# Optimization experiments

Hardware: AMD Instinct MI355X
Metric: run time of the kernel (lower is better)

Reference implementation:

```python
import jax, jax.numpy as jnp
import numpy as np

ALPHA = 0.2  # LeakyReLU negative slope
OUT_FEATURES = 128


def setup_inputs() -> dict:
    key = jax.random.key(0)
    k1, k2, k3 = jax.random.split(key, 3)
    B, N, F_in, F_out = 4, 4096, 128, OUT_FEATURES
    h = jax.random.normal(k1, (B, N, F_in), dtype=jnp.float32)
    # xavier_uniform with gain 1.414: bound = gain * sqrt(6/(fan_in+fan_out))
    bw = 1.414 * np.sqrt(6.0 / (F_in + F_out))
    W = jax.random.uniform(k2, (F_in, F_out), minval=-bw, maxval=bw, dtype=jnp.float32)
    ba = 1.414 * np.sqrt(6.0 / (2 * F_out + 1))
    a = jax.random.uniform(k3, (2 * F_out, 1), minval=-ba, maxval=ba, dtype=jnp.float32)
    return {"h": h, "W": W, "a": a}


def reference(h, W, a):
    # Wh: [B, N, F_out]
    Wh = jnp.einsum("bni,ij->bnj", h, W)
    a1 = a[:OUT_FEATURES, :]   # [F_out, 1]
    a2 = a[OUT_FEATURES:, :]   # [F_out, 1]
    Wh1 = jnp.einsum("bni,ij->bnj", Wh, a1)  # [B, N, 1]
    Wh2 = jnp.einsum("bni,ij->bnj", Wh, a2)  # [B, N, 1]
    # e: [B, N, N] via broadcast add of column + row vectors
    e = Wh1 + jnp.swapaxes(Wh2, 1, 2)
    e = jax.nn.leaky_relu(e, negative_slope=ALPHA)
    attention = jax.nn.softmax(e, axis=2)
    # dropout is identity in eval mode (p=0.0 / training=False)
    h_prime = jnp.einsum("bij,bjn->bin", attention, Wh)
    return jax.nn.elu(h_prime)
```

## Files before the change

### kernel.cpp

```cpp
#include <hip/hip_runtime.h>
#include <hip/hip_bf16.h>


#define ALPHA 0.2f
#define NN 4096
#define FD 128

typedef __attribute__((ext_vector_type(8))) short s8v;
typedef __attribute__((ext_vector_type(4))) float f4v;
typedef __attribute__((ext_vector_type(2))) unsigned int u2v;
typedef __attribute__((ext_vector_type(4))) unsigned int u4v;

__device__ __forceinline__ unsigned short f2bf(float x) {
  return (unsigned short)((__float_as_uint(x) + 0x8000u) >> 16);
}

__global__ __launch_bounds__(256, 4) void k1_gemm(
    const float* __restrict__ h, const float* __restrict__ W,
    const float* __restrict__ a,
    unsigned short* __restrict__ WhTt,
    float* __restrict__ s1g, float* __restrict__ Eg, float* __restrict__ Fg)
{
  __shared__ __align__(16) unsigned char wls[32768];
  const int tid = threadIdx.x;
  const int b = blockIdx.x >> 6;
  const int j0 = (blockIdx.x & 63) << 6;

#pragma unroll
  for (int it = 0; it < 16; ++it) {
    int cidx = it * 256 + tid;
    int i = cidx >> 5;
    int f0 = (cidx & 31) << 2;
    f4v v = *(const f4v*)(W + (size_t)cidx * 4);
#pragma unroll
    for (int e = 0; e < 4; ++e) {
      int f = f0 + e;
      int byte = f * 256 + (((i >> 3) ^ (f & 15)) << 4) + ((i & 7) << 1);
      *(unsigned short*)(wls + byte) = f2bf(v[e]);
    }
  }
  __syncthreads();

  const int w = tid >> 6, lane = tid & 63;
  const int quad = lane >> 4, lcol = lane & 15;
  const int jrow = j0 + 16 * w + lcol;

  f4v acc[8];
#pragma unroll
  for (int nt = 0; nt < 8; ++nt) acc[nt] = (f4v){0.f, 0.f, 0.f, 0.f};

#pragma unroll
  for (int kk = 0; kk < 4; ++kk) {
    const float* hp = h + (((size_t)(b * NN + jrow)) << 7) + (kk << 5) + (quad << 3);
    f4v v0 = *(const f4v*)hp;
    f4v v1 = *(const f4v*)(hp + 4);
    s8v af;
#pragma unroll
    for (int e = 0; e < 4; ++e) { af[e] = (short)f2bf(v0[e]); af[4+e] = (short)f2bf(v1[e]); }
#pragma unroll
    for (int nt = 0; nt < 8; ++nt) {
      int f = 16 * nt + lcol;
      int slot = ((kk << 2) + quad) ^ (f & 15);
      s8v bfr = *(const s8v*)(wls + (f << 8) + (slot << 4));
      acc[nt] = __builtin_amdgcn_mfma_f32_16x16x32_bf16(af, bfr, acc[nt], 0, 0, 0);
    }
  }

  float s1v[4] = {0,0,0,0}, s2v[4] = {0,0,0,0};
#pragma unroll
  for (int nt = 0; nt < 8; ++nt) {
    float a1 = a[16 * nt + lcol];
    float a2 = a[128 + 16 * nt + lcol];
#pragma unroll
    for (int r = 0; r < 4; ++r) { s1v[r] += acc[nt][r] * a1; s2v[r] += acc[nt][r] * a2; }
  }
#pragma unroll
  for (int r = 0; r < 4; ++r)
#pragma unroll
    for (int d = 1; d < 16; d <<= 1) {
      s1v[r] += __shfl_xor(s1v[r], d, 64);
      s2v[r] += __shfl_xor(s2v[r], d, 64);
    }
  if (lcol == 0) {
    int jb = b * NN + j0 + 16 * w + (quad << 2);
    *(f4v*)(s1g + jb) = (f4v){s1v[0], s1v[1], s1v[2], s1v[3]};
    f4v Ee, Ff;
#pragma unroll
    for (int r = 0; r < 4; ++r) {
      float d = s2v[r] - 8.0f;
      Ee[r] = __expf(d);
      Ff[r] = __expf(ALPHA * d);
    }
    *(f4v*)(Eg + jb) = Ee;
    *(f4v*)(Fg + jb) = Ff;
  }

  {
    const int c = j0 >> 8;
    const int octb = ((j0 & 255) >> 3) + 2 * w + (quad >> 1);
    const int eoff = (quad & 1) << 2;
#pragma unroll
    for (int nt = 0; nt < 8; ++nt) {
      int f = 16 * nt + lcol;
      unsigned u0 = __float_as_uint(acc[nt][0]) + 0x8000u;
      unsigned u1 = __float_as_uint(acc[nt][1]) + 0x8000u;
      unsigned u2 = __float_as_uint(acc[nt][2]) + 0x8000u;
      unsigned u3 = __float_as_uint(acc[nt][3]) + 0x8000u;
      u2v pk;
      pk[0] = (u0 >> 16) | (u1 & 0xFFFF0000u);
      pk[1] = (u2 >> 16) | (u3 & 0xFFFF0000u);
      size_t off = ((((size_t)(b * 16 + c) * 32 + octb) * 128 + f) << 3) + eoff;
      *(u2v*)(WhTt + off) = pk;
    }
  }
}

__global__ __launch_bounds__(256, 2) void k3_v5(
    const unsigned short* __restrict__ WhTt,
    const float* __restrict__ s1g,
    const float* __restrict__ Eg,
    const float* __restrict__ Fg,
    unsigned short* __restrict__ pO,
    float* __restrict__ pl)
{
  __shared__ __align__(16) unsigned char smem[20480];
  const int tid = threadIdx.x;
  const int w = tid >> 6, lane = tid & 63;
  const int quad = lane >> 4, lcol = lane & 15;
  const int blk = blockIdx.x;
  const int b = blk >> 7, rgb = (blk >> 3) & 15, jq = blk & 7;
  const int irow0 = rgb * 256 + w * 64;

  const unsigned short* whtb = WhTt + ((size_t)b << 19);
  const float* Egb = Eg + b * NN + (jq << 9);
  const float* Fgb = Fg + b * NN + (jq << 9);

  if (tid < 128) {
    f4v v = *(const f4v*)(Egb + tid * 4);
    *(f4v*)(smem + 16384 + tid * 16) = v;
  } else {
    f4v v = *(const f4v*)(Fgb + (tid - 128) * 4);
    *(f4v*)(smem + 18432 + (tid - 128) * 16) = v;
  }

  float rr[4];
#pragma unroll
  for (int mt = 0; mt < 4; ++mt) {
    float x = s1g[b * NN + irow0 + 16 * mt + lcol] + 8.0f;
    rr[mt] = __expf((ALPHA - 1.0f) * x);
  }

  auto tilePtr = [&](int s) -> const unsigned short* {
    int og0 = (jq << 6) + (s << 2);
    return whtb + (((size_t)(og0 >> 5)) << 15) + ((og0 & 31) << 10);
  };
  {
    const unsigned short* tp = tilePtr(0);
    u4v t0 = *(const u4v*)(tp + tid * 8);
    u4v t1 = *(const u4v*)(tp + 2048 + tid * 8);
    *(u4v*)(smem + tid * 16) = t0;
    *(u4v*)(smem + 4096 + tid * 16) = t1;
  }

  f4v acc[4][8], accL[4];
#pragma unroll
  for (int mt = 0; mt < 4; ++mt) {
    accL[mt] = (f4v){0.f, 0.f, 0.f, 0.f};
#pragma unroll
    for (int nt = 0; nt < 8; ++nt) acc[mt][nt] = (f4v){0.f, 0.f, 0.f, 0.f};
  }
  s8v ones;
  {
    short o = (lcol == 0) ? (short)0x3F80 : (short)0;
#pragma unroll
    for (int t = 0; t < 8; ++t) ones[t] = o;
  }

  const float* EFb = (const float*)(smem + 16384);

  for (int s = 0; s < 16; ++s) {
    __syncthreads();
    u4v tn0, tn1;
    if (s < 15) {
      const unsigned short* tp = tilePtr(s + 1);
      tn0 = *(const u4v*)(tp + tid * 8);
      tn1 = *(const u4v*)(tp + 2048 + tid * 8);
    }
    const unsigned char* buf = smem + ((s & 1) << 13);

    const int jloc = (s << 5) + (quad << 3);
    f4v Ea0 = *(const f4v*)(EFb + jloc);
    f4v Ea1 = *(const f4v*)(EFb + jloc + 4);
    f4v Fa0 = *(const f4v*)(EFb + 512 + jloc);
    f4v Fa1 = *(const f4v*)(EFb + 512 + jloc + 4);
    float Ev[8] = {Ea0[0], Ea0[1], Ea0[2], Ea0[3], Ea1[0], Ea1[1], Ea1[2], Ea1[3]};
    float Fv[8] = {Fa0[0], Fa0[1], Fa0[2], Fa0[3], Fa1[0], Fa1[1], Fa1[2], Fa1[3]};

    s8v bfr[8];
#pragma unroll
    for (int nt = 0; nt < 8; ++nt) {
      int f = (nt << 4) + lcol;
      bfr[nt] = *(const s8v*)(buf + (quad << 11) + (f << 4));
    }

    s8v af[4];
#pragma unroll
    for (int mt = 0; mt < 4; ++mt) {
      float R = rr[mt];
      u4v pk4;
#pragma unroll
      for (int t = 0; t < 8; t += 2) {
        float q0 = fmaxf(Ev[t], R * Fv[t]);
        float q1 = fmaxf(Ev[t + 1], R * Fv[t + 1]);
        unsigned u0 = __float_as_uint(q0) + 0x8000u;
        unsigned u1 = __float_as_uint(q1) + 0x8000u;
        pk4[t >> 1] = __builtin_amdgcn_perm(u1, u0, 0x07060302);
      }
      af[mt] = __builtin_bit_cast(s8v, pk4);
    }
#pragma unroll
    for (int nt = 0; nt < 8; ++nt)
#pragma unroll
      for (int mt = 0; mt < 4; ++mt)
        acc[mt][nt] = __builtin_amdgcn_mfma_f32_16x16x32_bf16(af[mt], bfr[nt], acc[mt][nt], 0, 0, 0);
#pragma unroll
    for (int mt = 0; mt < 4; ++mt)
      accL[mt] = __builtin_amdgcn_mfma_f32_16x16x32_bf16(af[mt], ones, accL[mt], 0, 0, 0);

    if (s < 15) {
      unsigned char* dst = smem + (((s + 1) & 1) << 13);
      *(u4v*)(dst + tid * 16) = tn0;
      *(u4v*)(dst + 4096 + tid * 16) = tn1;
    }
  }

  if (lcol == 0) {
#pragma unroll
    for (int mt = 0; mt < 4; ++mt)
#pragma unroll
      for (int r = 0; r < 4; ++r)
        pl[(size_t)blk * 256 + w * 64 + 16 * mt + (quad << 2) + r] = accL[mt][r];
  }
  unsigned short* po = pO + (size_t)blk * 32768;
#pragma unroll
  for (int mt = 0; mt < 4; ++mt)
#pragma unroll
    for (int nt = 0; nt < 8; ++nt) {
      unsigned u0 = __float_as_uint(acc[mt][nt][0]) + 0x8000u;
      unsigned u1 = __float_as_uint(acc[mt][nt][1]) + 0x8000u;
      unsigned u2 = __float_as_uint(acc[mt][nt][2]) + 0x8000u;
      unsigned u3 = __float_as_uint(acc[mt][nt][3]) + 0x8000u;
      u2v pk;
      pk[0] = (u0 >> 16) | (u1 & 0xFFFF0000u);
      pk[1] = (u2 >> 16) | (u3 & 0xFFFF0000u);
      int off = ((((w << 2) + mt) << 3) + nt) * 256 + (lane << 2);
      *(u2v*)(po + off) = pk;
    }
}

__global__ __launch_bounds__(256) void k4_comb(
    const unsigned short* __restrict__ pO, const float* __restrict__ pl,
    float* __restrict__ out)
{
  const int tid = threadIdx.x, blk = blockIdx.x;
  const int b = blk >> 7, chunk = (blk >> 1) & 63, sel = blk & 1;
  const int rgb = chunk >> 2, wv = chunk & 3;
  const int mt = tid >> 6, lane = tid & 63;
  const int quad = lane >> 4, lcol = lane & 15;
  const int kb = (b << 7) | (rgb << 3);

  float il[4];
#pragma unroll
  for (int r = 0; r < 4; ++r) {
    int rowloc = wv * 64 + 16 * mt + (quad << 2) + r;
    float l = 0.f;
#pragma unroll
    for (int q = 0; q < 8; ++q) l += pl[(size_t)(kb + q) * 256 + rowloc];
    il[r] = 1.0f / l;
  }

  const size_t rowg0 = ((size_t)b * NN + rgb * 256 + wv * 64 + 16 * mt + (quad << 2));
#pragma unroll
  for (int ntl = 0; ntl < 4; ++ntl) {
    const int nt = (sel << 2) + ntl;
    const int off = ((((wv << 2) + mt) << 3) + nt) * 256 + (lane << 2);
    float s0 = 0.f, s1 = 0.f, s2 = 0.f, s3 = 0.f;
#pragma unroll
    for (int q = 0; q < 8; ++q) {
      u2v pk = *(const u2v*)(pO + (size_t)(kb + q) * 32768 + off);
      s0 += __uint_as_float(pk[0] << 16);
      s1 += __uint_as_float(pk[0] & 0xFFFF0000u);
      s2 += __uint_as_float(pk[1] << 16);
      s3 += __uint_as_float(pk[1] & 0xFFFF0000u);
    }
    float v[4] = {s0 * il[0], s1 * il[1], s2 * il[2], s3 * il[3]};
#pragma unroll
    for (int r = 0; r < 4; ++r) {
      float x = v[r];
      x = x > 0.f ? x : (__expf(x) - 1.f);
      out[(rowg0 + r) * 128 + (nt << 4) + lcol] = x;
    }
  }
}

__global__ __launch_bounds__(512, 2) void k3_mono(
    const unsigned short* __restrict__ WhTt,
    const float* __restrict__ s1g,
    const float* __restrict__ Eg,
    const float* __restrict__ Fg,
    float* __restrict__ out)
{
  __shared__ __align__(16) unsigned char smem[33024];
  const int tid = threadIdx.x;
  const int kp = tid >> 6, lane = tid & 63;
  const int quad = lane >> 4, lcol = lane & 15;
  const int b = (blockIdx.x & 7) >> 1;
  const int i0 = ((((blockIdx.x & 1) << 5) | (blockIdx.x >> 3))) << 6;
  const int c0 = (blockIdx.x >> 3) & 15;
  const int oct = (kp << 2) + quad;

  float Ar[4], Br[4];
#pragma unroll
  for (int mt = 0; mt < 4; ++mt) {
    float x = s1g[b * NN + i0 + 16 * mt + lcol] + 8.0f;
    float m = fmaxf(x, ALPHA * x);
    Ar[mt] = __expf(x - m);
    Br[mt] = __expf(ALPHA * x - m);
  }

  f4v acc[4][8], accL[4];
#pragma unroll
  for (int mt = 0; mt < 4; ++mt) {
    accL[mt] = (f4v){0.f, 0.f, 0.f, 0.f};
#pragma unroll
    for (int nt = 0; nt < 8; ++nt) acc[mt][nt] = (f4v){0.f, 0.f, 0.f, 0.f};
  }
  s8v ones;
  {
    short o = (lcol == 0) ? (short)0x3F80 : (short)0;
#pragma unroll
    for (int t = 0; t < 8; ++t) ones[t] = o;
  }

  const unsigned short* whtb = WhTt + ((size_t)b << 19);
  const float* Egb = Eg + b * NN;
  const float* Fgb = Fg + b * NN;
  const int jw = oct << 3;

  f4v Ec0 = *(const f4v*)(Egb + (c0 << 8) + jw);
  f4v Ec1 = *(const f4v*)(Egb + (c0 << 8) + jw + 4);
  f4v Fc0 = *(const f4v*)(Fgb + (c0 << 8) + jw);
  f4v Fc1 = *(const f4v*)(Fgb + (c0 << 8) + jw + 4);

  for (int cc = 0; cc < 16; ++cc) {
    const int c = (cc + c0) & 15;
    const unsigned short* tile = whtb + ((size_t)c << 15) + (oct << 10);
    s8v bfr[8];
#pragma unroll
    for (int nt = 0; nt < 8; ++nt)
      bfr[nt] = *(const s8v*)(tile + (((nt << 4) + lcol) << 3));

    f4v En0, En1, Fn0, Fn1;
    if (cc < 15) {
      int jg = (((cc + 1 + c0) & 15) << 8) + jw;
      En0 = *(const f4v*)(Egb + jg); En1 = *(const f4v*)(Egb + jg + 4);
      Fn0 = *(const f4v*)(Fgb + jg); Fn1 = *(const f4v*)(Fgb + jg + 4);
    }

    float Ev[8] = {Ec0[0], Ec0[1], Ec0[2], Ec0[3], Ec1[0], Ec1[1], Ec1[2], Ec1[3]};
    float Fv[8] = {Fc0[0], Fc0[1], Fc0[2], Fc0[3], Fc1[0], Fc1[1], Fc1[2], Fc1[3]};

    s8v af[4];
#pragma unroll
    for (int mt = 0; mt < 4; ++mt) {
      float A = Ar[mt], Bc = Br[mt];
      u4v pk4;
#pragma unroll
      for (int t = 0; t < 8; t += 2) {
        float p0 = fmaxf(A * Ev[t], Bc * Fv[t]);
        float p1 = fmaxf(A * Ev[t + 1], Bc * Fv[t + 1]);
        unsigned u0 = __float_as_uint(p0) + 0x8000u;
        unsigned u1 = __float_as_uint(p1) + 0x8000u;
        pk4[t >> 1] = __builtin_amdgcn_perm(u1, u0, 0x07060302);
      }
      af[mt] = __builtin_bit_cast(s8v, pk4);
    }
#pragma unroll
    for (int nt = 0; nt < 8; ++nt)
#pragma unroll
      for (int mt = 0; mt < 4; ++mt)
        acc[mt][nt] = __builtin_amdgcn_mfma_f32_16x16x32_bf16(af[mt], bfr[nt], acc[mt][nt], 0, 0, 0);
#pragma unroll
    for (int mt = 0; mt < 4; ++mt)
      accL[mt] = __builtin_amdgcn_mfma_f32_16x16x32_bf16(af[mt], ones, accL[mt], 0, 0, 0);

    Ec0 = En0; Ec1 = En1; Fc0 = Fn0; Fc1 = Fn1;
  }

  float* hsum = (float*)smem;
  float* l_red = (float*)(smem + 32768);
#pragma unroll
  for (int t = 0; t < 4; ++t)
    *(f4v*)(hsum + tid * 16 + t * 4) = (f4v){0.f, 0.f, 0.f, 0.f};
  if (tid < 64) l_red[tid] = 0.f;
  __syncthreads();

#pragma unroll
  for (int mt = 0; mt < 4; ++mt) {
    if (lcol == 0) {
#pragma unroll
      for (int r = 0; r < 4; ++r)
        atomicAdd(&l_red[16 * mt + (quad << 2) + r], accL[mt][r]);
    }
#pragma unroll
    for (int nt = 0; nt < 8; ++nt)
#pragma unroll
      for (int r = 0; r < 4; ++r) {
        int row = 16 * mt + (quad << 2) + r;
        int f = (nt << 4) + lcol;
        int fx = (f + (quad << 3)) & 127;
        atomicAdd(&hsum[(row << 7) + fx], acc[mt][nt][r]);
      }
  }
  __syncthreads();

  {
    int r = tid >> 3;
    int f0 = (tid & 7) << 4;
    int off = ((r >> 2) & 3) << 3;
    float il = 1.0f / l_red[r];
    size_t o = (((size_t)b * NN + i0 + r) << 7) + f0;
#pragma unroll
    for (int t = 0; t < 4; ++t) {
      int fx = (f0 + 4 * t + off) & 127;
      f4v v = *(const f4v*)(hsum + (r << 7) + fx);
      f4v ov;
#pragma unroll
      for (int e = 0; e < 4; ++e) {
        float x = v[e] * il;
        ov[e] = x > 0.f ? x : (__expf(x) - 1.f);
      }
      *(f4v*)(out + o + 4 * t) = ov;
    }
  }
}

extern "C" void kernel_launch(void* const* d_in, const int* in_sizes, int n_in,
                              void* d_out, int out_size, void* d_ws, size_t ws_size,
                              hipStream_t stream) {
  const float* h = (const float*)d_in[0];
  const float* W = (const float*)d_in[1];
  const float* a = (const float*)d_in[2];
  float* out = (float*)d_out;
  unsigned char* ws = (unsigned char*)d_ws;

  unsigned short* WhTt = (unsigned short*)ws;
  float* s1g = (float*)(ws + 4194304);
  float* Eg  = (float*)(ws + 4259840);
  float* Fg  = (float*)(ws + 4325376);
  unsigned short* pO = (unsigned short*)(ws + 4390912);
  float* pl = (float*)(ws + 37945344);
  const size_t NEED_SPLIT = 38469632;
  const size_t NEED_MONO = 4390912;
  if (ws_size < NEED_MONO) return;

  hipLaunchKernelGGL(k1_gemm, dim3(256), dim3(256), 0, stream,
                     h, W, a, WhTt, s1g, Eg, Fg);
  if (ws_size >= NEED_SPLIT) {
    hipLaunchKernelGGL(k3_v5, dim3(512), dim3(256), 0, stream,
                       WhTt, s1g, Eg, Fg, pO, pl);
    hipLaunchKernelGGL(k4_comb, dim3(512), dim3(256), 0, stream,
                       pO, pl, out);
  } else {
    hipLaunchKernelGGL(k1_gemm, dim3(256), dim3(256), 0, stream,
                       h, W, a, WhTt, s1g, Eg, Fg);
    hipLaunchKernelGGL(k3_mono, dim3(256), dim3(512), 0, stream,
                       WhTt, s1g, Eg, Fg, out);
  }
}
```

Before: 102.5 us.

## Fuse split-K combine into attention kernel via per-group atomic counter barrier

The separate combine kernel is removed. Each attention block now bumps a per-row-group atomic counter, spins until all eight split blocks of its group finish, then reduces a slice of the partial outputs and softmax sums and writes the ELU result. The aim is to drop one kernel launch and its tail, at the cost of relying on all eight blocks of a group being co-resident. That residency is likely with 512 blocks at two per CU, and a bounded spin limits deadlock risk. The counter is reset by the first GEMM block each call.

```diff
diff --git a/kernel.cpp b/kernel.cpp
--- a/kernel.cpp
+++ b/kernel.cpp
@@ -19,12 +19,15 @@
     const float* __restrict__ h, const float* __restrict__ W,
     const float* __restrict__ a,
     unsigned short* __restrict__ WhTt,
-    float* __restrict__ s1g, float* __restrict__ Eg, float* __restrict__ Fg)
+    float* __restrict__ s1g, float* __restrict__ Eg, float* __restrict__ Fg,
+    int* cnt)
 {
   __shared__ __align__(16) unsigned char wls[32768];
   const int tid = threadIdx.x;
   const int b = blockIdx.x >> 6;
   const int j0 = (blockIdx.x & 63) << 6;
+
+  if (cnt && blockIdx.x == 0 && tid < 64) cnt[tid] = 0;
 
 #pragma unroll
   for (int it = 0; it < 16; ++it) {
@@ -115,13 +118,15 @@
   }
 }
 
-__global__ __launch_bounds__(256, 2) void k3_v5(
+__global__ __launch_bounds__(256, 2) void k3_v6(
     const unsigned short* __restrict__ WhTt,
     const float* __restrict__ s1g,
     const float* __restrict__ Eg,
     const float* __restrict__ Fg,
     unsigned short* __restrict__ pO,
-    float* __restrict__ pl)
+    float* __restrict__ pl,
+    int* __restrict__ cnt,
+    float* __restrict__ out)
 {
   __shared__ __align__(16) unsigned char smem[20480];
   const int tid = threadIdx.x;
@@ -256,49 +261,59 @@
       int off = ((((w << 2) + mt) << 3) + nt) * 256 + (lane << 2);
       *(u2v*)(po + off) = pk;
     }
-}
-
-__global__ __launch_bounds__(256) void k4_comb(
-    const unsigned short* __restrict__ pO, const float* __restrict__ pl,
-    float* __restrict__ out)
-{
-  const int tid = threadIdx.x, blk = blockIdx.x;
-  const int b = blk >> 7, chunk = (blk >> 1) & 63, sel = blk & 1;
-  const int rgb = chunk >> 2, wv = chunk & 3;
-  const int mt = tid >> 6, lane = tid & 63;
-  const int quad = lane >> 4, lcol = lane & 15;
-  const int kb = (b << 7) | (rgb << 3);
-
-  float il[4];
-#pragma unroll
-  for (int r = 0; r < 4; ++r) {
-    int rowloc = wv * 64 + 16 * mt + (quad << 2) + r;
-    float l = 0.f;
-#pragma unroll
-    for (int q = 0; q < 8; ++q) l += pl[(size_t)(kb + q) * 256 + rowloc];
-    il[r] = 1.0f / l;
-  }
-
-  const size_t rowg0 = ((size_t)b * NN + rgb * 256 + wv * 64 + 16 * mt + (quad << 2));
-#pragma unroll
-  for (int ntl = 0; ntl < 4; ++ntl) {
-    const int nt = (sel << 2) + ntl;
-    const int off = ((((wv << 2) + mt) << 3) + nt) * 256 + (lane << 2);
-    float s0 = 0.f, s1 = 0.f, s2 = 0.f, s3 = 0.f;
+
+  const int g = b * 16 + rgb;
+  __syncthreads();
+  if (tid == 0) {
+    __threadfence();
+    __hip_atomic_fetch_add(&cnt[g], 1, __ATOMIC_ACQ_REL, __HIP_MEMORY_SCOPE_AGENT);
+    int spin = 0;
+    while (__hip_atomic_load(&cnt[g], __ATOMIC_ACQUIRE, __HIP_MEMORY_SCOPE_AGENT) < 8
+           && spin < (1 << 20)) { __builtin_amdgcn_s_sleep(2); ++spin; }
+    __threadfence();
+  }
+  __syncthreads();
+
+  {
+    const int kb = (blk >> 3) << 3;
+    const int wsrc = jq >> 1;
+    const int mt0 = (jq & 1) << 1;
+    const int wsub = tid >> 6;
+    const int mt = mt0 + (wsub >> 1);
+    const int sel = wsub & 1;
+
+    const int rowloc = wsrc * 64 + mt * 16 + (quad << 2);
+    f4v lsum = (f4v){0.f, 0.f, 0.f, 0.f};
 #pragma unroll
     for (int q = 0; q < 8; ++q) {
-      u2v pk = *(const u2v*)(pO + (size_t)(kb + q) * 32768 + off);
-      s0 += __uint_as_float(pk[0] << 16);
-      s1 += __uint_as_float(pk[0] & 0xFFFF0000u);
-      s2 += __uint_as_float(pk[1] << 16);
-      s3 += __uint_as_float(pk[1] & 0xFFFF0000u);
-    }
-    float v[4] = {s0 * il[0], s1 * il[1], s2 * il[2], s3 * il[3]};
-#pragma unroll
-    for (int r = 0; r < 4; ++r) {
-      float x = v[r];
-      x = x > 0.f ? x : (__expf(x) - 1.f);
-      out[(rowg0 + r) * 128 + (nt << 4) + lcol] = x;
+      f4v lv = *(const f4v*)(pl + (size_t)(kb + q) * 256 + rowloc);
+      lsum[0] += lv[0]; lsum[1] += lv[1]; lsum[2] += lv[2]; lsum[3] += lv[3];
+    }
+    float il[4];
+#pragma unroll
+    for (int r = 0; r < 4; ++r) il[r] = 1.0f / lsum[r];
+
+    const size_t rowg0 = (size_t)b * NN + rgb * 256 + rowloc;
+#pragma unroll
+    for (int ntl = 0; ntl < 4; ++ntl) {
+      const int nt = (sel << 2) + ntl;
+      const int off = ((((wsrc << 2) + mt) << 3) + nt) * 256 + (lane << 2);
+      float s0 = 0.f, s1 = 0.f, s2 = 0.f, s3 = 0.f;
+#pragma unroll
+      for (int q = 0; q < 8; ++q) {
+        u2v pk = *(const u2v*)(pO + (size_t)(kb + q) * 32768 + off);
+        s0 += __uint_as_float(pk[0] << 16);
+        s1 += __uint_as_float(pk[0] & 0xFFFF0000u);
+        s2 += __uint_as_float(pk[1] << 16);
+        s3 += __uint_as_float(pk[1] & 0xFFFF0000u);
+      }
+      float v[4] = {s0 * il[0], s1 * il[1], s2 * il[2], s3 * il[3]};
+#pragma unroll
+      for (int r = 0; r < 4; ++r) {
+        float x = v[r];
+        x = x > 0.f ? x : (__expf(x) - 1.f);
+        out[(rowg0 + r) * 128 + (nt << 4) + lcol] = x;
+      }
     }
   }
 }
@@ -460,20 +475,19 @@
   float* Fg  = (float*)(ws + 4325376);
   unsigned short* pO = (unsigned short*)(ws + 4390912);
   float* pl = (float*)(ws + 37945344);
-  const size_t NEED_SPLIT = 38469632;
+  int* cnt = (int*)(ws + 38469632);
+  const size_t NEED_SPLIT = 38469888;
   const size_t NEED_MONO = 4390912;
   if (ws_size < NEED_MONO) return;
 
-  hipLaunchKernelGGL(k1_gemm, dim3(256), dim3(256), 0, stream,
-                     h, W, a, WhTt, s1g, Eg, Fg);
   if (ws_size >= NEED_SPLIT) {
-    hipLaunchKernelGGL(k3_v5, dim3(512), dim3(256), 0, stream,
-                       WhTt, s1g, Eg, Fg, pO, pl);
-    hipLaunchKernelGGL(k4_comb, dim3(512), dim3(256), 0, stream,
-                       pO, pl, out);
+    hipLaunchKernelGGL(k1_gemm, dim3(256), dim3(256), 0, stream,
+                       h, W, a, WhTt, s1g, Eg, Fg, cnt);
+    hipLaunchKernelGGL(k3_v6, dim3(512), dim3(256), 0, stream,
+                       WhTt, s1g, Eg, Fg, pO, pl, cnt, out);
   } else {
     hipLaunchKernelGGL(k1_gemm, dim3(256), dim3(256), 0, stream,
-                       h, W, a, WhTt, s1g, Eg, Fg);
+                       h, W, a, WhTt, s1g, Eg, Fg, (int*)nullptr);
     hipLaunchKernelGGL(k3_mono, dim3(256), dim3(512), 0, stream,
                        WhTt, s1g, Eg, Fg, out);
   }
```

Result: slower. 163.3 us (+59.4%).
